# Optimization experiments

Measured on AMD Instinct MI355X. Metric: run time of the kernel, lower is better.

The kernel has to match this reference:

```python
import jax, jax.numpy as jnp
import numpy as np

BG_OPACITY = 1e10  # background_opacity
BG_COLOR = 0.0     # bg_color = (0.0,)


def setup_inputs() -> dict:
    key = jax.random.key(0)
    k1, k2, k3, k4 = jax.random.split(key, 4)
    B, R, N, C = 8, 16384, 128, 3
    rays_densities = jax.random.uniform(k1, (B, R, N, 1), dtype=jnp.float32) * 2.0
    rays_features = jax.random.uniform(k2, (B, R, N, C), dtype=jnp.float32)
    # monotonically increasing sample depths along the ray
    steps = jax.random.uniform(k3, (B, R, N), dtype=jnp.float32) * 0.05 + 0.01
    ray_lengths = jnp.cumsum(steps, axis=-1) + 2.0
    ray_directions = jax.random.normal(k4, (B, R, 3), dtype=jnp.float32)
    return {
        "rays_densities": rays_densities,
        "rays_features": rays_features,
        "ray_lengths": ray_lengths,
        "ray_directions": ray_directions,
    }


def reference(rays_densities, rays_features, ray_lengths, ray_directions):
    # deltas between consecutive samples; last delta is the background opacity
    deltas = jnp.concatenate(
        [ray_lengths[..., 1:] - ray_lengths[..., :-1],
         jnp.full_like(ray_lengths[..., :1], BG_OPACITY)], axis=-1)
    dir_norm = jnp.linalg.norm(ray_directions, axis=-1)  # (B, R)
    deltas = deltas * dir_norm[..., None]
    dens = jax.nn.relu(rays_densities[..., 0])  # density_relu=True, bias=0
    weighted = deltas * dens  # (B, R, N)
    capped = 1.0 - jnp.exp(-weighted)  # exponential capping
    rays_opacities = 1.0 - jnp.exp(-jnp.cumsum(weighted, axis=-1))
    opacities = rays_opacities[..., -1:]  # (B, R, 1)
    # roll absorption by surface_thickness=1 and set leading entry to 1
    absorption = 1.0 - rays_opacities
    absorption_shifted = jnp.roll(absorption, 1, axis=-1).at[..., :1].set(1.0)
    weights = capped * absorption_shifted  # product weight function
    depths = jnp.sum(weights * ray_lengths, axis=-1, keepdims=True)
    features = jnp.einsum('brn,brnc->brc', weights, rays_features)
    # blend_output=False -> alpha = 1; bg_color scalar 0.0 broadcast
    features = features + (1.0 - opacities) * BG_COLOR
    return features, depths, opacities, weights
```

## Files before the change

kernel.cpp:

```cpp
#include <hip/hip_runtime.h>


#define BG_OPACITY_F 1e10f

typedef float floatx4 __attribute__((ext_vector_type(4)));

#define RSTRIDE 388

__global__ __launch_bounds__(256, 4) void ea_render_kernel(
    const float* __restrict__ dens,
    const float* __restrict__ feats,
    const float* __restrict__ lens,
    const float* __restrict__ dirs,
    float* __restrict__ out_feat,
    float* __restrict__ out_depth,
    float* __restrict__ out_opac,
    float* __restrict__ out_w,
    int n_rays)
{
    __shared__ __align__(16) float sfeat[16 * RSTRIDE];

    const int tid  = threadIdx.x;
    const int lane = tid & 63;
    const int t    = lane & 15;
    const int rb   = tid >> 4;
    const long ray0 = (long)blockIdx.x * 16;
    const long ray = (ray0 + rb < n_rays) ? (ray0 + rb) : (n_rays - 1);

    const long base = ray * 128;
    const int  n0   = t * 8;

    const float* fblock = feats + ray0 * 384;
    float4 fc[6];
    #pragma unroll
    for (int k = 0; k < 6; ++k) {
        const int c = k * 256 + tid;
        const bool ok = (ray0 + c / 96) < n_rays;
        fc[k] = ok ? *(const float4*)(fblock + (long)c * 4)
                   : make_float4(0.f, 0.f, 0.f, 0.f);
    }

    const float4 dA = *(const float4*)(dens + base + n0);
    const float4 dB = *(const float4*)(dens + base + n0 + 4);
    const float4 lA = *(const float4*)(lens + base + n0);
    const float4 lB = *(const float4*)(lens + base + n0 + 4);

    const float* dp = dirs + ray * 3;
    const float dx = dp[0], dy = dp[1], dz = dp[2];
    const float dn = sqrtf(dx * dx + dy * dy + dz * dz);

    const float l[8]  = {lA.x, lA.y, lA.z, lA.w, lB.x, lB.y, lB.z, lB.w};
    const float dv[8] = {dA.x, dA.y, dA.z, dA.w, dB.x, dB.y, dB.z, dB.w};

    const float lnext = __shfl_down(lA.x, 1, 64);

    float w[8];
    #pragma unroll
    for (int i = 0; i < 7; ++i)
        w[i] = (l[i + 1] - l[i]) * dn * fmaxf(dv[i], 0.0f);
    const float delta7 = (t == 15) ? BG_OPACITY_F : (lnext - l[7]);
    w[7] = delta7 * dn * fmaxf(dv[7], 0.0f);
    const float w7s = (t == 15) ? 0.0f : w[7];

    const float s = w[0] + w[1] + w[2] + w[3] + w[4] + w[5] + w[6] + w7s;

    float inc = s;
    #pragma unroll
    for (int off = 1; off < 16; off <<= 1) {
        const float u = __shfl_up(inc, off, 64);
        if (t >= off) inc += u;
    }
    const float excl = inc - s;

    float a = __expf(-excl);
    float wgt[8];
    #pragma unroll
    for (int i = 0; i < 8; ++i) {
        const float ei = __expf(-w[i]);
        wgt[i] = (1.0f - ei) * a;
        a *= ei;
    }

    const floatx4 wv0 = {wgt[0], wgt[1], wgt[2], wgt[3]};
    const floatx4 wv1 = {wgt[4], wgt[5], wgt[6], wgt[7]};
    __builtin_nontemporal_store(wv0, (floatx4*)(out_w + base + n0));
    __builtin_nontemporal_store(wv1, (floatx4*)(out_w + base + n0 + 4));

    if (t == 15) {
        out_opac[ray] = 1.0f - __expf(-(inc + w[7]));
    }

    #pragma unroll
    for (int k = 0; k < 6; ++k) {
        const int c   = k * 256 + tid;
        const int r   = c / 96;
        const int rem = c - r * 96;
        const int tq  = rem / 6;
        const int iq  = rem - tq * 6;
        *(float4*)&sfeat[r * RSTRIDE + tq * 24 + iq * 4] = fc[k];
    }
    __syncthreads();

    const float* myf = &sfeat[rb * RSTRIDE + t * 24];
    const float4 q0 = *(const float4*)(myf +  0);
    const float4 q1 = *(const float4*)(myf +  4);
    const float4 q2 = *(const float4*)(myf +  8);
    const float4 q3 = *(const float4*)(myf + 12);
    const float4 q4 = *(const float4*)(myf + 16);
    const float4 q5 = *(const float4*)(myf + 20);
    const float f[24] = {q0.x, q0.y, q0.z, q0.w, q1.x, q1.y, q1.z, q1.w,
                         q2.x, q2.y, q2.z, q2.w, q3.x, q3.y, q3.z, q3.w,
                         q4.x, q4.y, q4.z, q4.w, q5.x, q5.y, q5.z, q5.w};

    float pd = 0.0f, fr = 0.0f, fg = 0.0f, fb = 0.0f;
    #pragma unroll
    for (int i = 0; i < 8; ++i) {
        pd += wgt[i] * l[i];
        fr += wgt[i] * f[3 * i + 0];
        fg += wgt[i] * f[3 * i + 1];
        fb += wgt[i] * f[3 * i + 2];
    }

    #pragma unroll
    for (int off = 8; off; off >>= 1) {
        pd += __shfl_xor(pd, off, 64);
        fr += __shfl_xor(fr, off, 64);
        fg += __shfl_xor(fg, off, 64);
        fb += __shfl_xor(fb, off, 64);
    }

    if (t == 0) {
        out_feat[ray * 3 + 0] = fr;
        out_feat[ray * 3 + 1] = fg;
        out_feat[ray * 3 + 2] = fb;
        out_depth[ray] = pd;
    }
}

extern "C" void kernel_launch(void* const* d_in, const int* in_sizes, int n_in,
                              void* d_out, int out_size, void* d_ws, size_t ws_size,
                              hipStream_t stream) {
    const float* dens  = (const float*)d_in[0];
    const float* feats = (const float*)d_in[1];
    const float* lens  = (const float*)d_in[2];
    const float* dirs  = (const float*)d_in[3];

    const int n_rays = in_sizes[3] / 3;

    float* out = (float*)d_out;
    float* out_feat  = out;
    float* out_depth = out + (long)n_rays * 3;
    float* out_opac  = out + (long)n_rays * 4;
    float* out_w     = out + (long)n_rays * 5;

    const int blocks = (n_rays + 15) / 16;
    ea_render_kernel<<<blocks, 256, 0, stream>>>(
        dens, feats, lens, dirs, out_feat, out_depth, out_opac, out_w, n_rays);
}
```

Before: 381.1 us.

## Make kernel persistent with register double-buffered prefetch of next tile

Turns the one-tile-per-block kernel into a grid-stride persistent kernel capped at 1024 blocks. Each block prefetches the next tile's features, densities, lengths and directions into registers while it computes the current tile, so global load latency overlaps with compute. The trade-off is higher register pressure from the duplicate buffers, an extra barrier per tile, and fewer resident waves to hide latency in a memory-bound kernel. The feature dot products are also rewritten to index the loaded vectors directly instead of going through a temporary array.

```diff
diff --git a/kernel.cpp b/kernel.cpp
--- a/kernel.cpp
+++ b/kernel.cpp
@@ -24,116 +24,144 @@
     const int lane = tid & 63;
     const int t    = lane & 15;
     const int rb   = tid >> 4;
-    const long ray0 = (long)blockIdx.x * 16;
-    const long ray = (ray0 + rb < n_rays) ? (ray0 + rb) : (n_rays - 1);
+    const int n_tiles = (n_rays + 15) >> 4;
 
-    const long base = ray * 128;
-    const int  n0   = t * 8;
+    float4 fc[6],  nfc[6];
+    float4 dA, dB, lA, lB, ndA, ndB, nlA, nlB;
+    float  dx, dy, dz, ndx, ndy, ndz;
 
-    const float* fblock = feats + ray0 * 384;
-    float4 fc[6];
-    #pragma unroll
-    for (int k = 0; k < 6; ++k) {
-        const int c = k * 256 + tid;
-        const bool ok = (ray0 + c / 96) < n_rays;
-        fc[k] = ok ? *(const float4*)(fblock + (long)c * 4)
-                   : make_float4(0.f, 0.f, 0.f, 0.f);
-    }
+    auto ISSUE = [&](long tk, float4* FC, float4& DA, float4& DB,
+                     float4& LA, float4& LB,
+                     float& DX, float& DY, float& DZ) {
+        const long ray0 = tk << 4;
+        const long ray  = (ray0 + rb < n_rays) ? (ray0 + rb) : (n_rays - 1);
+        const long base = ray * 128;
+        const int  n0   = t * 8;
+        #pragma unroll
+        for (int k = 0; k < 6; ++k) {
+            const int c = k * 256 + tid;
+            long r = ray0 + c / 96;
+            if (r >= n_rays) r = n_rays - 1;
+            FC[k] = *(const float4*)(feats + r * 384 + (long)(c % 96) * 4);
+        }
+        DA = *(const float4*)(dens + base + n0);
+        DB = *(const float4*)(dens + base + n0 + 4);
+        LA = *(const float4*)(lens + base + n0);
+        LB = *(const float4*)(lens + base + n0 + 4);
+        const float* dp = dirs + ray * 3;
+        DX = dp[0]; DY = dp[1]; DZ = dp[2];
+    };
 
-    const float4 dA = *(const float4*)(dens + base + n0);
-    const float4 dB = *(const float4*)(dens + base + n0 + 4);
-    const float4 lA = *(const float4*)(lens + base + n0);
-    const float4 lB = *(const float4*)(lens + base + n0 + 4);
+    long tile = blockIdx.x;
+    if (tile >= n_tiles) return;
+    const long step = gridDim.x;
 
-    const float* dp = dirs + ray * 3;
-    const float dx = dp[0], dy = dp[1], dz = dp[2];
-    const float dn = sqrtf(dx * dx + dy * dy + dz * dz);
+    ISSUE(tile, fc, dA, dB, lA, lB, dx, dy, dz);
 
-    const float l[8]  = {lA.x, lA.y, lA.z, lA.w, lB.x, lB.y, lB.z, lB.w};
-    const float dv[8] = {dA.x, dA.y, dA.z, dA.w, dB.x, dB.y, dB.z, dB.w};
+    for (; tile < n_tiles; tile += step) {
+        #pragma unroll
+        for (int k = 0; k < 6; ++k) {
+            const int c   = k * 256 + tid;
+            const int r   = c / 96;
+            const int rem = c - r * 96;
+            const int tq  = rem / 6;
+            const int iq  = rem - tq * 6;
+            *(float4*)&sfeat[r * RSTRIDE + tq * 24 + iq * 4] = fc[k];
+        }
+        __syncthreads();
 
-    const float lnext = __shfl_down(lA.x, 1, 64);
+        const long next = tile + step;
+        if (next < n_tiles)
+            ISSUE(next, nfc, ndA, ndB, nlA, nlB, ndx, ndy, ndz);
 
-    float w[8];
-    #pragma unroll
-    for (int i = 0; i < 7; ++i)
-        w[i] = (l[i + 1] - l[i]) * dn * fmaxf(dv[i], 0.0f);
-    const float delta7 = (t == 15) ? BG_OPACITY_F : (lnext - l[7]);
-    w[7] = delta7 * dn * fmaxf(dv[7], 0.0f);
-    const float w7s = (t == 15) ? 0.0f : w[7];
+        const long ray0 = tile << 4;
+        const long ray  = (ray0 + rb < n_rays) ? (ray0 + rb) : (n_rays - 1);
+        const long base = ray * 128;
+        const int  n0   = t * 8;
 
-    const float s = w[0] + w[1] + w[2] + w[3] + w[4] + w[5] + w[6] + w7s;
+        const float dn = sqrtf(dx * dx + dy * dy + dz * dz);
+        const float l[8]  = {lA.x, lA.y, lA.z, lA.w, lB.x, lB.y, lB.z, lB.w};
+        const float dv[8] = {dA.x, dA.y, dA.z, dA.w, dB.x, dB.y, dB.z, dB.w};
 
-    float inc = s;
-    #pragma unroll
-    for (int off = 1; off < 16; off <<= 1) {
-        const float u = __shfl_up(inc, off, 64);
-        if (t >= off) inc += u;
-    }
-    const float excl = inc - s;
+        const float lnext = __shfl_down(lA.x, 1, 64);
 
-    float a = __expf(-excl);
-    float wgt[8];
-    #pragma unroll
-    for (int i = 0; i < 8; ++i) {
-        const float ei = __expf(-w[i]);
-        wgt[i] = (1.0f - ei) * a;
-        a *= ei;
-    }
+        float w[8];
+        #pragma unroll
+        for (int i = 0; i < 7; ++i)
+            w[i] = (l[i + 1] - l[i]) * dn * fmaxf(dv[i], 0.0f);
+        const float delta7 = (t == 15) ? BG_OPACITY_F : (lnext - l[7]);
+        w[7] = delta7 * dn * fmaxf(dv[7], 0.0f);
+        const float w7s = (t == 15) ? 0.0f : w[7];
 
-    const floatx4 wv0 = {wgt[0], wgt[1], wgt[2], wgt[3]};
-    const floatx4 wv1 = {wgt[4], wgt[5], wgt[6], wgt[7]};
-    __builtin_nontemporal_store(wv0, (floatx4*)(out_w + base + n0));
-    __builtin_nontemporal_store(wv1, (floatx4*)(out_w + base + n0 + 4));
+        const float s = w[0] + w[1] + w[2] + w[3] + w[4] + w[5] + w[6] + w7s;
 
-    if (t == 15) {
-        out_opac[ray] = 1.0f - __expf(-(inc + w[7]));
-    }
+        float inc = s;
+        #pragma unroll
+        for (int off = 1; off < 16; off <<= 1) {
+            const float u = __shfl_up(inc, off, 64);
+            if (t >= off) inc += u;
+        }
+        const float excl = inc - s;
 
-    #pragma unroll
-    for (int k = 0; k < 6; ++k) {
-        const int c   = k * 256 + tid;
-        const int r   = c / 96;
-        const int rem = c - r * 96;
-        const int tq  = rem / 6;
-        const int iq  = rem - tq * 6;
-        *(float4*)&sfeat[r * RSTRIDE + tq * 24 + iq * 4] = fc[k];
-    }
-    __syncthreads();
+        float a = __expf(-excl);
+        float wgt[8];
+        #pragma unroll
+        for (int i = 0; i < 8; ++i) {
+            const float ei = __expf(-w[i]);
+            wgt[i] = (1.0f - ei) * a;
+            a *= ei;
+        }
 
-    const float* myf = &sfeat[rb * RSTRIDE + t * 24];
-    const float4 q0 = *(const float4*)(myf +  0);
-    const float4 q1 = *(const float4*)(myf +  4);
-    const float4 q2 = *(const float4*)(myf +  8);
-    const float4 q3 = *(const float4*)(myf + 12);
-    const float4 q4 = *(const float4*)(myf + 16);
-    const float4 q5 = *(const float4*)(myf + 20);
-    const float f[24] = {q0.x, q0.y, q0.z, q0.w, q1.x, q1.y, q1.z, q1.w,
-                         q2.x, q2.y, q2.z, q2.w, q3.x, q3.y, q3.z, q3.w,
-                         q4.x, q4.y, q4.z, q4.w, q5.x, q5.y, q5.z, q5.w};
+        const floatx4 wv0 = {wgt[0], wgt[1], wgt[2], wgt[3]};
+        const floatx4 wv1 = {wgt[4], wgt[5], wgt[6], wgt[7]};
+        __builtin_nontemporal_store(wv0, (floatx4*)(out_w + base + n0));
+        __builtin_nontemporal_store(wv1, (floatx4*)(out_w + base + n0 + 4));
 
-    float pd = 0.0f, fr = 0.0f, fg = 0.0f, fb = 0.0f;
-    #pragma unroll
-    for (int i = 0; i < 8; ++i) {
-        pd += wgt[i] * l[i];
-        fr += wgt[i] * f[3 * i + 0];
-        fg += wgt[i] * f[3 * i + 1];
-        fb += wgt[i] * f[3 * i + 2];
-    }
+        if (t == 15) {
+            out_opac[ray] = 1.0f - __expf(-(inc + w[7]));
+        }
 
-    #pragma unroll
-    for (int off = 8; off; off >>= 1) {
-        pd += __shfl_xor(pd, off, 64);
-        fr += __shfl_xor(fr, off, 64);
-        fg += __shfl_xor(fg, off, 64);
-        fb += __shfl_xor(fb, off, 64);
-    }
+        const float* myf = &sfeat[rb * RSTRIDE + t * 24];
+        const float4 q0 = *(const float4*)(myf +  0);
+        const float4 q1 = *(const float4*)(myf +  4);
+        const float4 q2 = *(const float4*)(myf +  8);
+        const float4 q3 = *(const float4*)(myf + 12);
+        const float4 q4 = *(const float4*)(myf + 16);
+        const float4 q5 = *(const float4*)(myf + 20);
 
-    if (t == 0) {
-        out_feat[ray * 3 + 0] = fr;
-        out_feat[ray * 3 + 1] = fg;
-        out_feat[ray * 3 + 2] = fb;
-        out_depth[ray] = pd;
+        float pd = 0.0f, fr = 0.0f, fg = 0.0f, fb = 0.0f;
+        #pragma unroll
+        for (int i = 0; i < 8; ++i) pd += wgt[i] * l[i];
+        fr = wgt[0]*q0.x + wgt[1]*q0.w + wgt[2]*q1.z + wgt[3]*q2.y
+           + wgt[4]*q3.x + wgt[5]*q3.w + wgt[6]*q4.z + wgt[7]*q5.y;
+        fg = wgt[0]*q0.y + wgt[1]*q1.x + wgt[2]*q1.w + wgt[3]*q2.z
+           + wgt[4]*q3.y + wgt[5]*q4.x + wgt[6]*q4.w + wgt[7]*q5.z;
+        fb = wgt[0]*q0.z + wgt[1]*q1.y + wgt[2]*q2.x + wgt[3]*q2.w
+           + wgt[4]*q3.z + wgt[5]*q4.y + wgt[6]*q5.x + wgt[7]*q5.w;
+
+        #pragma unroll
+        for (int off = 8; off; off >>= 1) {
+            pd += __shfl_xor(pd, off, 64);
+            fr += __shfl_xor(fr, off, 64);
+            fg += __shfl_xor(fg, off, 64);
+            fb += __shfl_xor(fb, off, 64);
+        }
+
+        if (t == 0) {
+            out_feat[ray * 3 + 0] = fr;
+            out_feat[ray * 3 + 1] = fg;
+            out_feat[ray * 3 + 2] = fb;
+            out_depth[ray] = pd;
+        }
+
+        __syncthreads();
+
+        if (next < n_tiles) {
+            #pragma unroll
+            for (int k = 0; k < 6; ++k) fc[k] = nfc[k];
+            dA = ndA; dB = ndB; lA = nlA; lB = nlB;
+            dx = ndx; dy = ndy; dz = ndz;
+        }
     }
 }
 
@@ -153,7 +181,8 @@
     float* out_opac  = out + (long)n_rays * 4;
     float* out_w     = out + (long)n_rays * 5;
 
-    const int blocks = (n_rays + 15) / 16;
+    const int n_tiles = (n_rays + 15) / 16;
+    const int blocks  = n_tiles < 1024 ? n_tiles : 1024;
     ea_render_kernel<<<blocks, 256, 0, stream>>>(
         dens, feats, lens, dirs, out_feat, out_depth, out_opac, out_w, n_rays);
 }
```

Result: slower. 455.7 us (+19.6%).
